# Optimization experiments

Hardware: AMD Instinct MI355X
Metric: run time of the kernel (lower is better)

## Reference

```python
import jax, jax.numpy as jnp
import numpy as np

FEAT = 32      # feature_dim
NA = 64        # num_azimuths
NE = 32        # num_elevations - 2 (interior elevation rings)
N = 2_000_000  # number of query points
NORMALIZED = False


def setup_inputs() -> dict:
    key = jax.random.key(0)
    k1, k2, k3 = jax.random.split(key, 3)
    u = jax.random.uniform(k1, (2, N), dtype=jnp.float32)
    # azimuth in [-pi, pi), elevation in [-pi/2, pi/2]
    az = u[0] * (2.0 * np.pi) * (1.0 - 1e-7) - np.pi
    el = u[1] * np.pi - np.pi / 2
    points_to_interp = jnp.stack([az, el])
    grid_values = jax.random.normal(k2, (FEAT, NA, NE), dtype=jnp.float32) * 0.1
    grid_values_poles = jax.random.normal(k3, (FEAT, 2), dtype=jnp.float32) * 0.1
    return {
        "points_to_interp": points_to_interp,
        "grid_values": grid_values,
        "grid_values_poles": grid_values_poles,
    }


def _slerp(f1, f2, theta, omega, normalized):
    # spherical linear interpolation weights; omega is a static python float
    w1 = jnp.sin(omega - theta)
    w2 = jnp.sin(theta)
    if normalized:
        s = w1 + w2
        w1 = w1 / s
        w2 = w2 / s
    else:
        so = np.sin(omega)
        w1 = w1 / so
        w2 = w2 / so
    return w1 * f1 + w2 * f2


def reference(points_to_interp, grid_values, grid_values_poles):
    F, na, ne = grid_values.shape
    # static grid ticks (buffers in the torch module)
    ticks_az = jnp.asarray(np.linspace(-np.pi, np.pi, na + 1)[:-1], jnp.float32)
    ticks_el = jnp.asarray(np.linspace(-np.pi / 2, np.pi / 2, ne + 2)[1:-1], jnp.float32)
    omega_az = 2.0 * np.pi / na            # azimuth tick spacing
    omega_el = np.pi / (ne + 1)            # elevation tick spacing (incl. poles)

    az = points_to_interp[0]
    el = points_to_interp[1]

    # torch.bucketize(right=False) == searchsorted side='left'
    ar = jnp.searchsorted(ticks_az, az, side="left")
    al = ar - 1
    ar = jnp.where(ar >= na, 0, ar)        # azimuth wraps around
    al = jnp.where(al < 0, na - 1, al)     # torch negative index wrap

    er = jnp.searchsorted(ticks_el, el, side="left")
    south = er == 0                        # below lowest interior ring
    north = er == ne                       # above highest interior ring
    eil = jnp.clip(er - 1, 0, ne - 1)      # lower ring index (clamped)
    eir = jnp.clip(er, 0, ne - 1)          # upper ring index (clamped)

    # azimuth slerp on the lower and upper rings (4 gathers of [F, N])
    theta_az = az - ticks_az[al]
    f_b = _slerp(grid_values[:, al, eil], grid_values[:, ar, eil], theta_az, omega_az, NORMALIZED)
    f_t = _slerp(grid_values[:, al, eir], grid_values[:, ar, eir], theta_az, omega_az, NORMALIZED)

    # pole regions: blend ring value with pole feature.
    # slerp(a, b, theta, omega) == slerp(b, a, omega - theta, omega), so the
    # north-pole branch slerp(pole, f_top_ring, pi/2 - el) equals
    # slerp(f_top_ring, pole, el - ticks_el[ne-1]) with the same omega_el.
    f1 = jnp.where(south, grid_values_poles[:, 0:1], f_b)
    f2 = jnp.where(north, grid_values_poles[:, 1:2], f_t)
    base = jnp.where(south, -np.pi / 2, ticks_el[eil])
    theta_el = el - base
    return _slerp(f1, f2, theta_el, omega_el, NORMALIZED)
```

## Files before the change

### kernel.cpp

```cpp
#include <hip/hip_runtime.h>
#include <hip/hip_fp16.h>

namespace {

constexpr int kFeat = 32;
constexpr int kNA = 64;
constexpr int kNE = 32;
constexpr int kGridElems = kFeat * kNA * kNE;
constexpr int kPoleElems = kFeat * 2;
constexpr int kCols = kNA * kNE;
constexpr int kColS = kCols;
constexpr int kColN = kCols + 1;
constexpr int kTotCols = kCols + 2;

constexpr float kPi  = 3.14159265358979323846f;
constexpr float kPi2 = 1.57079632679489661923f;
constexpr float kOmegaAz = 0.09817477042468103f;
constexpr float kOmegaEl = 0.09519977738150889f;
constexpr float kInvOmegaAz = 10.18591635788130f;
constexpr float kInvOmegaEl = 10.50422624406509f;
constexpr float kInvSinAz = 10.20229703f;
constexpr float kInvSinEl = 10.52010966f;

typedef float vfloat4 __attribute__((ext_vector_type(4)));

__global__ __launch_bounds__(256) void transpose_grid_h(
    const float* __restrict__ g, const float* __restrict__ poles,
    __half* __restrict__ gt) {
  int idx = blockIdx.x * 256 + threadIdx.x;
  if (idx < kGridElems) {
    int f = idx >> 11;
    int ae = idx & 2047;
    gt[ae * kFeat + f] = __float2half(g[idx]);
  }
  if (idx < kPoleElems) {
    int f = idx >> 1;
    int p = idx & 1;
    gt[(kCols + p) * kFeat + f] = __float2half(poles[idx]);
  }
}

struct PointSetup {
  int col_bl, col_br, col_tl, col_tr;
  float a1, a2, b1, b2;
};

__device__ __forceinline__ PointSetup setup_point(float az, float el) {
  PointSetup s;
  float ta = (az + kPi) * kInvOmegaAz;
  int ar0 = (int)ceilf(ta);
  int al = ar0 - 1;
  int ar = (ar0 >= kNA) ? 0 : ar0;
  if (al < 0) al = kNA - 1;
  float theta_a = az - (-kPi + (float)al * kOmegaAz);
  float w1a = __sinf(kOmegaAz - theta_a) * kInvSinAz;
  float w2a = __sinf(theta_a) * kInvSinAz;

  float ue = (el + kPi2) * kInvOmegaEl;
  int er = (int)ceilf(ue) - 1;
  er = min(max(er, 0), kNE);
  bool south = (er == 0);
  bool north = (er == kNE);
  int eil = min(max(er - 1, 0), kNE - 1);
  int eir = min(er, kNE - 1);
  float base = south ? -kPi2 : (-kPi2 + (float)(eil + 1) * kOmegaEl);
  float theta_e = el - base;
  float w1e = __sinf(kOmegaEl - theta_e) * kInvSinEl;
  float w2e = __sinf(theta_e) * kInvSinEl;

  s.col_bl = al * kNE + eil;
  s.col_br = ar * kNE + eil;
  s.col_tl = al * kNE + eir;
  s.col_tr = ar * kNE + eir;
  s.a1 = w1e * w1a; s.a2 = w1e * w2a;
  s.b1 = w2e * w1a; s.b2 = w2e * w2a;
  if (south) {
    s.col_bl = kColS; s.col_br = kColS;
    s.a1 = 0.5f * w1e; s.a2 = s.a1;
  }
  if (north) {
    s.col_tl = kColN; s.col_tr = kColN;
    s.b1 = 0.5f * w2e; s.b2 = s.b1;
  }
  return s;
}

constexpr int kTile = 256;
constexpr int kTileFloats = kFeat * kTile;

__global__ __launch_bounds__(256) void interp_t(
    const float* __restrict__ pts, const __half* __restrict__ gt,
    float* __restrict__ out, int n) {
  __shared__ float tile[kTileFloats];
  const int base = blockIdx.x * kTile;
  const int rem = min(kTile, n - base);
  const size_t sn = (size_t)n;
  const int t = threadIdx.x;

  int   pidx[4];
  float azv[4], elv[4];
#pragma unroll
  for (int c = 0; c < 4; ++c) {
    int L = t + 256 * c;
    int p = L >> 2;
    pidx[c] = p;
    if (p < rem) {
      int i = base + p;
      azv[c] = pts[i];
      elv[c] = pts[n + i];
    } else {
      azv[c] = 0.f; elv[c] = 0.f;
    }
  }

#pragma unroll
  for (int c = 0; c < 4; ++c) {
    int L = t + 256 * c;
    int p = pidx[c];
    int j = L & 3;
    if (p < rem) {
      PointSetup s = setup_point(azv[c], elv[c]);
      union H8 { uint4 u; __half2 h[4]; };
      H8 bl, br, tl, tr;
      const int off = j * 8;
      bl.u = *(const uint4*)(gt + s.col_bl * kFeat + off);
      br.u = *(const uint4*)(gt + s.col_br * kFeat + off);
      tl.u = *(const uint4*)(gt + s.col_tl * kFeat + off);
      tr.u = *(const uint4*)(gt + s.col_tr * kFeat + off);

      const int colw = p ^ (j << 3);
      float* dst = tile + (8 * j) * kTile + colw;
#pragma unroll
      for (int q = 0; q < 4; ++q) {
        float2 vbl = __half22float2(bl.h[q]);
        float2 vbr = __half22float2(br.h[q]);
        float2 vtl = __half22float2(tl.h[q]);
        float2 vtr = __half22float2(tr.h[q]);
        dst[(2 * q + 0) * kTile] =
            s.a1 * vbl.x + s.a2 * vbr.x + s.b1 * vtl.x + s.b2 * vtr.x;
        dst[(2 * q + 1) * kTile] =
            s.a1 * vbl.y + s.a2 * vbr.y + s.b1 * vtl.y + s.b2 * vtr.y;
      }
    }
  }

  __syncthreads();

  if (rem == kTile) {
#pragma unroll
    for (int r = 0; r < 8; ++r) {
      int u = t + 256 * r;
      int row = u >> 6;
      int c4 = (u & 63) * 4;
      int swz = c4 ^ ((row >> 3) << 3);
      vfloat4 v = *(const vfloat4*)(tile + row * kTile + swz);
      __builtin_nontemporal_store(
          v, (vfloat4*)(out + (size_t)row * sn + base + c4));
    }
  } else {
    for (int r = 0; r < 8; ++r) {
      int u = t + 256 * r;
      int row = u >> 6;
      int c4 = (u & 63) * 4;
      int jrow = row >> 3;
      float* o = out + (size_t)row * sn + base;
      for (int e = 0; e < 4; ++e) {
        int p = c4 + e;
        if (p < rem) o[p] = tile[row * kTile + (p ^ (jrow << 3))];
      }
    }
  }
}

__global__ __launch_bounds__(256) void interp_d(
    const float* __restrict__ pts, const float* __restrict__ g,
    const float* __restrict__ poles, float* __restrict__ out, int n) {
  int i = blockIdx.x * 256 + threadIdx.x;
  if (i >= n) return;
  float az = pts[i];
  float el = pts[n + i];
  PointSetup s = setup_point(az, el);

  float a1 = s.a1, a2 = s.a2, b1 = s.b1, b2 = s.b2;
  float pw0 = 0.0f, pw1 = 0.0f;
  if (s.col_bl == kColS) { pw0 = a1 + a2; a1 = 0.0f; a2 = 0.0f; }
  if (s.col_tl == kColN) { pw1 = b1 + b2; b1 = 0.0f; b2 = 0.0f; }

  const float* gbl = g + (s.col_bl < kCols ? s.col_bl : 0);
  const float* gbr = g + (s.col_br < kCols ? s.col_br : 0);
  const float* gtl = g + (s.col_tl < kCols ? s.col_tl : 0);
  const float* gtr = g + (s.col_tr < kCols ? s.col_tr : 0);
  size_t sn = (size_t)n;
#pragma unroll 8
  for (int f = 0; f < kFeat; ++f) {
    float v = a1 * gbl[f * kCols] + a2 * gbr[f * kCols]
            + b1 * gtl[f * kCols] + b2 * gtr[f * kCols]
            + pw0 * poles[f * 2 + 0] + pw1 * poles[f * 2 + 1];
    out[(size_t)f * sn + i] = v;
  }
}

}

extern "C" void kernel_launch(void* const* d_in, const int* in_sizes, int n_in,
                              void* d_out, int out_size, void* d_ws, size_t ws_size,
                              hipStream_t stream) {
  (void)n_in; (void)out_size;
  const float* pts   = (const float*)d_in[0];
  const float* grid  = (const float*)d_in[1];
  const float* poles = (const float*)d_in[2];
  float* out = (float*)d_out;
  int n = in_sizes[0] / 2;

  size_t need = (size_t)(kTotCols * kFeat) * sizeof(__half);
  if (ws_size >= need) {
    __half* gt = (__half*)d_ws;
    transpose_grid_h<<<(kGridElems + 255) / 256, 256, 0, stream>>>(grid, poles, gt);
    int blocks = (n + kTile - 1) / kTile;
    interp_t<<<blocks, 256, 0, stream>>>(pts, gt, out, n);
  } else {
    int blocks = (n + 255) / 256;
    interp_d<<<blocks, 256, 0, stream>>>(pts, grid, poles, out, n);
  }
}
```

Before: 301.5 us.

## Assign one point per thread, drop LDS swizzle and nontemporal stores

Each thread now handles one whole point, loading all 32 fp16 features of its four grid columns itself, instead of four threads each taking 8 features of one point. This removes the four-fold repetition of the per-point setup (trig and index maths) and the staged point loads. It also drops the XOR swizzle in the shared-memory tile and replaces the nontemporal output stores with ordinary vector stores. In exchange each thread holds more registers and issues 16 wide gathers, and the unswizzled layout may change shared-memory bank behaviour.

New measurement: 314.1 us. 1.04x slower.

```diff
diff --git a/kernel.cpp b/kernel.cpp
--- a/kernel.cpp
+++ b/kernel.cpp
@@ -21,8 +21,6 @@
 constexpr float kInvOmegaEl = 10.50422624406509f;
 constexpr float kInvSinAz = 10.20229703f;
 constexpr float kInvSinEl = 10.52010966f;
-
-typedef float vfloat4 __attribute__((ext_vector_type(4)));
 
 __global__ __launch_bounds__(256) void transpose_grid_h(
     const float* __restrict__ g, const float* __restrict__ poles,
@@ -88,7 +86,7 @@
 constexpr int kTile = 256;
 constexpr int kTileFloats = kFeat * kTile;
 
-__global__ __launch_bounds__(256) void interp_t(
+__global__ __launch_bounds__(256) void interp_o(
     const float* __restrict__ pts, const __half* __restrict__ gt,
     float* __restrict__ out, int n) {
   __shared__ float tile[kTileFloats];
@@ -97,48 +95,39 @@
   const size_t sn = (size_t)n;
   const int t = threadIdx.x;
 
-  int   pidx[4];
-  float azv[4], elv[4];
-#pragma unroll
-  for (int c = 0; c < 4; ++c) {
-    int L = t + 256 * c;
-    int p = L >> 2;
-    pidx[c] = p;
-    if (p < rem) {
-      int i = base + p;
-      azv[c] = pts[i];
-      elv[c] = pts[n + i];
-    } else {
-      azv[c] = 0.f; elv[c] = 0.f;
-    }
-  }
-
-#pragma unroll
-  for (int c = 0; c < 4; ++c) {
-    int L = t + 256 * c;
-    int p = pidx[c];
-    int j = L & 3;
-    if (p < rem) {
-      PointSetup s = setup_point(azv[c], elv[c]);
-      union H8 { uint4 u; __half2 h[4]; };
-      H8 bl, br, tl, tr;
-      const int off = j * 8;
-      bl.u = *(const uint4*)(gt + s.col_bl * kFeat + off);
-      br.u = *(const uint4*)(gt + s.col_br * kFeat + off);
-      tl.u = *(const uint4*)(gt + s.col_tl * kFeat + off);
-      tr.u = *(const uint4*)(gt + s.col_tr * kFeat + off);
-
-      const int colw = p ^ (j << 3);
-      float* dst = tile + (8 * j) * kTile + colw;
-#pragma unroll
-      for (int q = 0; q < 4; ++q) {
-        float2 vbl = __half22float2(bl.h[q]);
-        float2 vbr = __half22float2(br.h[q]);
-        float2 vtl = __half22float2(tl.h[q]);
-        float2 vtr = __half22float2(tr.h[q]);
-        dst[(2 * q + 0) * kTile] =
+  if (t < rem) {
+    const int i = base + t;
+    const float az = pts[i];
+    const float el = pts[n + i];
+    PointSetup s = setup_point(az, el);
+
+    const uint4* cbl = (const uint4*)(gt + s.col_bl * kFeat);
+    const uint4* cbr = (const uint4*)(gt + s.col_br * kFeat);
+    const uint4* ctl = (const uint4*)(gt + s.col_tl * kFeat);
+    const uint4* ctr = (const uint4*)(gt + s.col_tr * kFeat);
+
+    union H8 { uint4 u; __half2 h[4]; };
+    H8 bl[4], br[4], tl[4], tr[4];
+#pragma unroll
+    for (int q = 0; q < 4; ++q) {
+      bl[q].u = cbl[q];
+      br[q].u = cbr[q];
+      tl[q].u = ctl[q];
+      tr[q].u = ctr[q];
+    }
+
+#pragma unroll
+    for (int q = 0; q < 4; ++q) {
+#pragma unroll
+      for (int h = 0; h < 4; ++h) {
+        float2 vbl = __half22float2(bl[q].h[h]);
+        float2 vbr = __half22float2(br[q].h[h]);
+        float2 vtl = __half22float2(tl[q].h[h]);
+        float2 vtr = __half22float2(tr[q].h[h]);
+        const int f = 8 * q + 2 * h;
+        tile[(f + 0) * kTile + t] =
             s.a1 * vbl.x + s.a2 * vbr.x + s.b1 * vtl.x + s.b2 * vtr.x;
-        dst[(2 * q + 1) * kTile] =
+        tile[(f + 1) * kTile + t] =
             s.a1 * vbl.y + s.a2 * vbr.y + s.b1 * vtl.y + s.b2 * vtr.y;
       }
     }
@@ -152,21 +141,18 @@
       int u = t + 256 * r;
       int row = u >> 6;
       int c4 = (u & 63) * 4;
-      int swz = c4 ^ ((row >> 3) << 3);
-      vfloat4 v = *(const vfloat4*)(tile + row * kTile + swz);
-      __builtin_nontemporal_store(
-          v, (vfloat4*)(out + (size_t)row * sn + base + c4));
+      uint4 v = *(const uint4*)(tile + row * kTile + c4);
+      *(uint4*)(out + (size_t)row * sn + base + c4) = v;
     }
   } else {
     for (int r = 0; r < 8; ++r) {
       int u = t + 256 * r;
       int row = u >> 6;
       int c4 = (u & 63) * 4;
-      int jrow = row >> 3;
       float* o = out + (size_t)row * sn + base;
       for (int e = 0; e < 4; ++e) {
         int p = c4 + e;
-        if (p < rem) o[p] = tile[row * kTile + (p ^ (jrow << 3))];
+        if (p < rem) o[p] = tile[row * kTile + p];
       }
     }
   }
@@ -217,7 +203,7 @@
     __half* gt = (__half*)d_ws;
     transpose_grid_h<<<(kGridElems + 255) / 256, 256, 0, stream>>>(grid, poles, gt);
     int blocks = (n + kTile - 1) / kTile;
-    interp_t<<<blocks, 256, 0, stream>>>(pts, gt, out, n);
+    interp_o<<<blocks, 256, 0, stream>>>(pts, gt, out, n);
   } else {
     int blocks = (n + 255) / 256;
     interp_d<<<blocks, 256, 0, stream>>>(pts, grid, poles, out, n);
```
